# Performance work log

Hardware: AMD Instinct MI355X
Metric: run time of the kernel (lower is better)

## Reference

```python
import jax, jax.numpy as jnp
import numpy as np

B, C, L = 16, 256, 2048


def setup_inputs() -> dict:
    key = jax.random.key(0)
    ks = jax.random.split(key, 7)
    s = 0.05
    return {
        "x": jax.random.normal(ks[0], (B, C, L), dtype=jnp.float32),
        "W_theta": jax.random.normal(ks[1], (C, C), dtype=jnp.float32) * s,
        "b_theta": jax.random.normal(ks[2], (C,), dtype=jnp.float32) * s,
        "W_phi": jax.random.normal(ks[3], (C, C), dtype=jnp.float32) * s,
        "b_phi": jax.random.normal(ks[4], (C,), dtype=jnp.float32) * s,
        "W_g": jax.random.normal(ks[5], (C, C), dtype=jnp.float32) * s,
        "b_g": jax.random.normal(ks[6], (C,), dtype=jnp.float32) * s,
    }


def reference(x, W_theta, b_theta, W_phi, b_phi, W_g, b_g):
    # x: [B, C, L]; 1x1 Conv1d == linear over channel dim: out[b,o,l] = W[o,c] x[b,c,l] + b[o]
    q = jnp.einsum('oc,bcl->bol', W_theta, x) + b_theta[None, :, None]  # [B,C,L]
    k = jnp.einsum('oc,bcl->bol', W_phi, x) + b_phi[None, :, None]
    v = jnp.einsum('oc,bcl->bol', W_g, x) + b_g[None, :, None]
    num_c = x.shape[1]
    # scores[b,i,j] = sum_c q[b,c,i] * k[b,c,j]
    scores = jnp.einsum('bci,bcj->bij', q, k) / jnp.sqrt(jnp.float32(num_c))  # [B,L,L]
    attn = jax.nn.softmax(scores, axis=-1)
    # out[b,i,c] = sum_j attn[b,i,j] v[b,c,j]; then permute back to [B,C,L]
    attn_out = jnp.einsum('bij,bcj->bci', attn, v)  # [B,C,L]
    return x + attn_out
```

## Files before the change

### kernel.cpp

```cpp
#include <hip/hip_runtime.h>
#include <math.h>

#define B_ 16
#define C_ 256
#define L_ 2048

using short8 = __attribute__((ext_vector_type(8))) short;
using f32x4  = __attribute__((ext_vector_type(4))) float;

__device__ __forceinline__ unsigned short f2bf(float f) {
  unsigned u = __float_as_uint(f);
  return (unsigned short)((u + 0x7FFFu + ((u >> 16) & 1u)) >> 16);
}

__device__ __forceinline__ void gload16(const void* src, void* dst) {
  __builtin_amdgcn_global_load_lds(
      (const __attribute__((address_space(1))) unsigned int*)src,
      (__attribute__((address_space(3))) unsigned int*)dst, 16, 0, 0);
}

__global__ __launch_bounds__(256) void convert_w(const float* __restrict__ wt,
                                                 const float* __restrict__ wp,
                                                 const float* __restrict__ wg,
                                                 unsigned short* __restrict__ dst) {
  int i = blockIdx.x * 256 + threadIdx.x;
  dst[i]          = f2bf(wt[i]);
  dst[65536 + i]  = f2bf(wp[i]);
  dst[131072 + i] = f2bf(wg[i]);
}

__global__ __launch_bounds__(256, 2) void proj_kernel(
    const float* __restrict__ x, const unsigned short* __restrict__ wbf,
    const float* __restrict__ bth, const float* __restrict__ bph,
    const float* __restrict__ bg,
    unsigned short* __restrict__ qT, unsigned short* __restrict__ kT,
    unsigned short* __restrict__ vv)
{
  const int tid  = threadIdx.x;
  const int w    = tid >> 6;
  const int lane = tid & 63;
  const int r    = lane & 15;
  const int g    = lane >> 4;
  const int l0   = blockIdx.x * 64;
  const int b    = blockIdx.y;
  const int p    = blockIdx.z;

  __shared__ unsigned short xs[64 * 64];
  __shared__ unsigned short wsd[256 * 64];

  const unsigned short* wsrc = wbf + p * 65536;

  f32x4 acc[4][4];
#pragma unroll
  for (int mi = 0; mi < 4; ++mi)
#pragma unroll
    for (int ni = 0; ni < 4; ++ni) acc[mi][ni] = f32x4{0.f, 0.f, 0.f, 0.f};

  for (int ks = 0; ks < 4; ++ks) {
    __syncthreads();
#pragma unroll
    for (int it = 0; it < 8; ++it) {
      int d  = it * 256 + w * 64 + lane;
      int o  = d >> 3;
      int cs = d & 7;
      const unsigned short* src = wsrc + o * C_ + ks * 64 + ((cs ^ (o & 7)) << 3);
      gload16(src, (void*)(wsd + (size_t)(it * 256 + w * 64) * 8));
    }
#pragma unroll
    for (int it = 0; it < 16; ++it) {
      int l = (tid & 15) + 16 * (it & 3);
      int c = (tid >> 4) + 16 * (it >> 2);
      float xvv = x[((size_t)b * C_ + ks * 64 + c) * L_ + l0 + l];
      xs[l * 64 + (((c >> 3) ^ (l & 7)) << 3) + (c & 7)] = f2bf(xvv);
    }
    __syncthreads();

#pragma unroll
    for (int kk2 = 0; kk2 < 2; ++kk2) {
      short8 xf[4], wf[4];
#pragma unroll
      for (int i = 0; i < 4; ++i) {
        int lrow = 16 * i + r;
        xf[i] = *(const short8*)(xs + lrow * 64 + (((kk2 * 4 + g) ^ (lrow & 7)) << 3));
        int orow = 64 * w + 16 * i + r;
        wf[i] = *(const short8*)(wsd + orow * 64 + (((kk2 * 4 + g) ^ (orow & 7)) << 3));
      }
      if (p < 2) {
#pragma unroll
        for (int mi = 0; mi < 4; ++mi)
#pragma unroll
          for (int ni = 0; ni < 4; ++ni)
            acc[mi][ni] = __builtin_amdgcn_mfma_f32_16x16x32_bf16(xf[mi], wf[ni], acc[mi][ni], 0, 0, 0);
      } else {
#pragma unroll
        for (int mi = 0; mi < 4; ++mi)
#pragma unroll
          for (int ni = 0; ni < 4; ++ni)
            acc[mi][ni] = __builtin_amdgcn_mfma_f32_16x16x32_bf16(wf[mi], xf[ni], acc[mi][ni], 0, 0, 0);
      }
    }
  }

  if (p < 2) {
    unsigned short* dst = (p == 0) ? qT : kT;
    const float* bias   = (p == 0) ? bth : bph;
    const float scale   = (p == 0) ? 0.09016844005556021f : 1.0f;
#pragma unroll
    for (int ni = 0; ni < 4; ++ni) {
      int o    = 64 * w + 16 * ni + r;
      float bv = bias[o];
#pragma unroll
      for (int mi = 0; mi < 4; ++mi)
#pragma unroll
        for (int rr = 0; rr < 4; ++rr) {
          int l = l0 + 16 * mi + 4 * g + rr;
          dst[((size_t)b * L_ + l) * C_ + o] = f2bf((acc[mi][ni][rr] + bv) * scale);
        }
    }
  } else {
#pragma unroll
    for (int mi = 0; mi < 4; ++mi)
#pragma unroll
      for (int rr = 0; rr < 4; ++rr) {
        int o    = 64 * w + 16 * mi + 4 * g + rr;
        float bv = bg[o];
#pragma unroll
        for (int ni = 0; ni < 4; ++ni) {
          int l = l0 + 16 * ni + r;
          vv[((size_t)b * C_ + o) * L_ + l] = f2bf(acc[mi][ni][rr] + bv);
        }
      }
  }
}

__global__ __launch_bounds__(256, 2) void attn_kernel(
    const unsigned short* __restrict__ qT, const unsigned short* __restrict__ kT,
    const unsigned short* __restrict__ vv,
    const float* __restrict__ x, float* __restrict__ out)
{
  const int tid  = threadIdx.x;
  const int w    = tid >> 6;
  const int lane = tid & 63;
  const int r    = lane & 15;
  const int g    = lane >> 4;

  int wg = ((blockIdx.x & 7) << 6) | (blockIdx.x >> 3);
  const int i0 = (wg & 31) * 64;
  const int b  = wg >> 5;

  __shared__ unsigned short kls[64 * 256];
  __shared__ unsigned short vls[256 * 64];
  __shared__ unsigned short pls[64 * 64];
  __shared__ float lsums[64];

  short8 qf[8];
  const int qrow = i0 + 16 * w + r;
#pragma unroll
  for (int kk = 0; kk < 8; ++kk)
    qf[kk] = *(const short8*)(qT + ((size_t)b * L_ + qrow) * C_ + kk * 32 + 8 * g);

  f32x4 oacc[4][4];
#pragma unroll
  for (int mi = 0; mi < 4; ++mi)
#pragma unroll
    for (int nf = 0; nf < 4; ++nf) oacc[mi][nf] = f32x4{0.f, 0.f, 0.f, 0.f};
  float lsum[4] = {0.f, 0.f, 0.f, 0.f};

  const unsigned short* kTb = kT + (size_t)b * L_ * C_;
  const unsigned short* vvb = vv + (size_t)b * C_ * L_;

  for (int jt = 0; jt < 32; ++jt) {
    const int j0 = jt * 64;
    __syncthreads();
#pragma unroll
    for (int it = 0; it < 8; ++it) {
      int d   = it * 256 + w * 64 + lane;
      int row = d >> 5;
      int cs  = d & 31;
      const unsigned short* src = kTb + (size_t)(j0 + row) * C_ + ((cs ^ (row & 7)) << 3);
      gload16(src, (void*)(kls + (size_t)(it * 256 + w * 64) * 8));
    }
#pragma unroll
    for (int it = 0; it < 8; ++it) {
      int d   = it * 256 + w * 64 + lane;
      int row = d >> 3;
      int cs  = d & 7;
      const unsigned short* src = vvb + (size_t)row * L_ + j0 + ((cs ^ (row & 7)) << 3);
      gload16(src, (void*)(vls + (size_t)(it * 256 + w * 64) * 8));
    }
    __syncthreads();

    f32x4 sacc[4];
#pragma unroll
    for (int ni = 0; ni < 4; ++ni) sacc[ni] = f32x4{0.f, 0.f, 0.f, 0.f};
#pragma unroll
    for (int kk = 0; kk < 8; ++kk) {
#pragma unroll
      for (int ni = 0; ni < 4; ++ni) {
        int jrow = 16 * ni + r;
        short8 kf = *(const short8*)(kls + jrow * 256 + (((4 * kk + g) ^ (jrow & 7)) << 3));
        sacc[ni] = __builtin_amdgcn_mfma_f32_16x16x32_bf16(qf[kk], kf, sacc[ni], 0, 0, 0);
      }
    }

#pragma unroll
    for (int ni = 0; ni < 4; ++ni) {
#pragma unroll
      for (int rr = 0; rr < 4; ++rr) {
        float pv = exp2f(sacc[ni][rr]);
        lsum[rr] += pv;
        int irow = 16 * w + 4 * g + rr;
        int j    = r + 16 * ni;
        pls[irow * 64 + (((j >> 3) ^ (irow & 7)) << 3) + (j & 7)] = f2bf(pv);
      }
    }
    __syncthreads();

#pragma unroll
    for (int kk2 = 0; kk2 < 2; ++kk2) {
      short8 pf[4];
#pragma unroll
      for (int mi = 0; mi < 4; ++mi) {
        int irow = 16 * mi + r;
        pf[mi] = *(const short8*)(pls + irow * 64 + (((4 * kk2 + g) ^ (irow & 7)) << 3));
      }
#pragma unroll
      for (int nf = 0; nf < 4; ++nf) {
        int crow = 64 * w + 16 * nf + r;
        short8 vf = *(const short8*)(vls + crow * 64 + (((4 * kk2 + g) ^ (crow & 7)) << 3));
#pragma unroll
        for (int mi = 0; mi < 4; ++mi)
          oacc[mi][nf] = __builtin_amdgcn_mfma_f32_16x16x32_bf16(pf[mi], vf, oacc[mi][nf], 0, 0, 0);
      }
    }
  }

#pragma unroll
  for (int off = 1; off < 16; off <<= 1)
#pragma unroll
    for (int rr = 0; rr < 4; ++rr) lsum[rr] += __shfl_xor(lsum[rr], off);
  if (r == 0) {
    f32x4 t{lsum[0], lsum[1], lsum[2], lsum[3]};
    *(f32x4*)(lsums + 16 * w + 4 * g) = t;
  }
  __syncthreads();

#pragma unroll
  for (int mi = 0; mi < 4; ++mi) {
    f32x4 ls = *(const f32x4*)(lsums + 16 * mi + 4 * g);
    f32x4 linv;
#pragma unroll
    for (int rr = 0; rr < 4; ++rr) linv[rr] = 1.0f / ls[rr];
#pragma unroll
    for (int nf = 0; nf < 4; ++nf) {
      int c = 64 * w + 16 * nf + r;
      size_t base = ((size_t)b * C_ + c) * L_ + i0 + 16 * mi + 4 * g;
      f32x4 xv = *(const f32x4*)(x + base);
      f32x4 ov;
#pragma unroll
      for (int rr = 0; rr < 4; ++rr) ov[rr] = xv[rr] + oacc[mi][nf][rr] * linv[rr];
      *(f32x4*)(out + base) = ov;
    }
  }
}

extern "C" void kernel_launch(void* const* d_in, const int* in_sizes, int n_in,
                              void* d_out, int out_size, void* d_ws, size_t ws_size,
                              hipStream_t stream) {
  (void)in_sizes; (void)n_in; (void)out_size; (void)ws_size;
  const float* x   = (const float*)d_in[0];
  const float* wt  = (const float*)d_in[1];
  const float* bt  = (const float*)d_in[2];
  const float* wp  = (const float*)d_in[3];
  const float* bp  = (const float*)d_in[4];
  const float* wg  = (const float*)d_in[5];
  const float* bgg = (const float*)d_in[6];
  float* out = (float*)d_out;

  char* ws = (char*)d_ws;
  unsigned short* wbf = (unsigned short*)ws;
  unsigned short* qT  = (unsigned short*)(ws + 393216);
  unsigned short* kT  = (unsigned short*)(ws + 393216 + 16777216);
  unsigned short* vv  = (unsigned short*)(ws + 393216 + 2 * 16777216);

  convert_w<<<dim3(256), dim3(256), 0, stream>>>(wt, wp, wg, wbf);
  proj_kernel<<<dim3(32, 16, 3), dim3(256), 0, stream>>>(x, wbf, bt, bp, bgg, qT, kT, vv);
  attn_kernel<<<dim3(512), dim3(256), 0, stream>>>(qT, kT, vv, x, out);
}
```

Before: 140.1 us.

## Switch attention to 32x32x16 MFMA, prefetch K tiles, load V directly

Rewrites the attention kernel to use 32x32x16 bf16 MFMA tiles, with each wave computing a 32x32 score block split over i and j halves. The next K tile is prefetched into LDS while the P·V product runs. V fragments are now read straight from global memory into registers, which drops the V LDS buffer and its staging. This cuts LDS traffic and synchronization per tile. In exchange it uses more registers for Q fragments and accumulators, and the global V reads now sit on the critical path.

```diff
diff --git a/kernel.cpp b/kernel.cpp
--- a/kernel.cpp
+++ b/kernel.cpp
@@ -7,6 +7,8 @@
 
 using short8 = __attribute__((ext_vector_type(8))) short;
 using f32x4  = __attribute__((ext_vector_type(4))) float;
+using f32x16 = __attribute__((ext_vector_type(16))) float;
+typedef unsigned int uint;
 
 __device__ __forceinline__ unsigned short f2bf(float f) {
   unsigned u = __float_as_uint(f);
@@ -141,127 +143,140 @@
   const int tid  = threadIdx.x;
   const int w    = tid >> 6;
   const int lane = tid & 63;
-  const int r    = lane & 15;
-  const int g    = lane >> 4;
+  const int l31  = lane & 31;
+  const int hi   = lane >> 5;
+  const int ih   = w >> 1;
+  const int jh   = w & 1;
 
   int wg = ((blockIdx.x & 7) << 6) | (blockIdx.x >> 3);
   const int i0 = (wg & 31) * 64;
   const int b  = wg >> 5;
 
   __shared__ unsigned short kls[64 * 256];
-  __shared__ unsigned short vls[256 * 64];
   __shared__ unsigned short pls[64 * 64];
-  __shared__ float lsums[64];
-
-  short8 qf[8];
-  const int qrow = i0 + 16 * w + r;
-#pragma unroll
-  for (int kk = 0; kk < 8; ++kk)
-    qf[kk] = *(const short8*)(qT + ((size_t)b * L_ + qrow) * C_ + kk * 32 + 8 * g);
-
-  f32x4 oacc[4][4];
-#pragma unroll
-  for (int mi = 0; mi < 4; ++mi)
-#pragma unroll
-    for (int nf = 0; nf < 4; ++nf) oacc[mi][nf] = f32x4{0.f, 0.f, 0.f, 0.f};
-  float lsum[4] = {0.f, 0.f, 0.f, 0.f};
+  __shared__ float lsums2[2][64];
+
+  short8 qf[16];
+  const unsigned short* qrow_p = qT + ((size_t)b * L_ + i0 + 32 * ih + l31) * C_;
+#pragma unroll
+  for (int ks = 0; ks < 16; ++ks)
+    qf[ks] = *(const short8*)(qrow_p + ks * 16 + 8 * hi);
+
+  f32x16 oacc[2][2];
+#pragma unroll
+  for (int it = 0; it < 2; ++it)
+#pragma unroll
+    for (int ct = 0; ct < 2; ++ct)
+#pragma unroll
+      for (int e = 0; e < 16; ++e) oacc[it][ct][e] = 0.f;
+  float lsum = 0.f;
 
   const unsigned short* kTb = kT + (size_t)b * L_ * C_;
   const unsigned short* vvb = vv + (size_t)b * C_ * L_;
+
+#pragma unroll
+  for (int it = 0; it < 8; ++it) {
+    int d   = it * 256 + w * 64 + lane;
+    int row = d >> 5;
+    int cs  = d & 31;
+    gload16(kTb + (size_t)row * C_ + ((cs ^ (row & 7)) << 3),
+            (void*)(kls + (size_t)(it * 256 + w * 64) * 8));
+  }
 
   for (int jt = 0; jt < 32; ++jt) {
     const int j0 = jt * 64;
     __syncthreads();
-#pragma unroll
-    for (int it = 0; it < 8; ++it) {
-      int d   = it * 256 + w * 64 + lane;
-      int row = d >> 5;
-      int cs  = d & 31;
-      const unsigned short* src = kTb + (size_t)(j0 + row) * C_ + ((cs ^ (row & 7)) << 3);
-      gload16(src, (void*)(kls + (size_t)(it * 256 + w * 64) * 8));
-    }
-#pragma unroll
-    for (int it = 0; it < 8; ++it) {
-      int d   = it * 256 + w * 64 + lane;
-      int row = d >> 3;
-      int cs  = d & 7;
-      const unsigned short* src = vvb + (size_t)row * L_ + j0 + ((cs ^ (row & 7)) << 3);
-      gload16(src, (void*)(vls + (size_t)(it * 256 + w * 64) * 8));
+
+    f32x16 sacc;
+#pragma unroll
+    for (int e = 0; e < 16; ++e) sacc[e] = 0.f;
+    const int jrow = l31 + 32 * jh;
+#pragma unroll
+    for (int ks = 0; ks < 16; ++ks) {
+      short8 kf = *(const short8*)(kls + jrow * 256 + (((2 * ks + hi) ^ (jrow & 7)) << 3));
+      sacc = __builtin_amdgcn_mfma_f32_32x32x16_bf16(kf, qf[ks], sacc, 0, 0, 0);
+    }
+
+    {
+      const int i = l31 + 32 * ih;
+#pragma unroll
+      for (int q = 0; q < 4; ++q) {
+        float p0 = exp2f(sacc[4 * q + 0]);
+        float p1 = exp2f(sacc[4 * q + 1]);
+        float p2 = exp2f(sacc[4 * q + 2]);
+        float p3 = exp2f(sacc[4 * q + 3]);
+        lsum += (p0 + p1) + (p2 + p3);
+        uint2 d2;
+        d2.x = (uint)f2bf(p0) | ((uint)f2bf(p1) << 16);
+        d2.y = (uint)f2bf(p2) | ((uint)f2bf(p3) << 16);
+        int slot = (4 * jh + q) ^ (i & 7);
+        *(uint2*)(pls + i * 64 + slot * 8 + 4 * hi) = d2;
+      }
     }
     __syncthreads();
 
-    f32x4 sacc[4];
-#pragma unroll
-    for (int ni = 0; ni < 4; ++ni) sacc[ni] = f32x4{0.f, 0.f, 0.f, 0.f};
-#pragma unroll
-    for (int kk = 0; kk < 8; ++kk) {
-#pragma unroll
-      for (int ni = 0; ni < 4; ++ni) {
-        int jrow = 16 * ni + r;
-        short8 kf = *(const short8*)(kls + jrow * 256 + (((4 * kk + g) ^ (jrow & 7)) << 3));
-        sacc[ni] = __builtin_amdgcn_mfma_f32_16x16x32_bf16(qf[kk], kf, sacc[ni], 0, 0, 0);
-      }
-    }
-
-#pragma unroll
-    for (int ni = 0; ni < 4; ++ni) {
-#pragma unroll
-      for (int rr = 0; rr < 4; ++rr) {
-        float pv = exp2f(sacc[ni][rr]);
-        lsum[rr] += pv;
-        int irow = 16 * w + 4 * g + rr;
-        int j    = r + 16 * ni;
-        pls[irow * 64 + (((j >> 3) ^ (irow & 7)) << 3) + (j & 7)] = f2bf(pv);
-      }
-    }
-    __syncthreads();
-
-#pragma unroll
-    for (int kk2 = 0; kk2 < 2; ++kk2) {
-      short8 pf[4];
-#pragma unroll
-      for (int mi = 0; mi < 4; ++mi) {
-        int irow = 16 * mi + r;
-        pf[mi] = *(const short8*)(pls + irow * 64 + (((4 * kk2 + g) ^ (irow & 7)) << 3));
-      }
-#pragma unroll
-      for (int nf = 0; nf < 4; ++nf) {
-        int crow = 64 * w + 16 * nf + r;
-        short8 vf = *(const short8*)(vls + crow * 64 + (((4 * kk2 + g) ^ (crow & 7)) << 3));
-#pragma unroll
-        for (int mi = 0; mi < 4; ++mi)
-          oacc[mi][nf] = __builtin_amdgcn_mfma_f32_16x16x32_bf16(pf[mi], vf, oacc[mi][nf], 0, 0, 0);
-      }
+    if (jt < 31) {
+#pragma unroll
+      for (int it = 0; it < 8; ++it) {
+        int d   = it * 256 + w * 64 + lane;
+        int row = d >> 5;
+        int cs  = d & 31;
+        gload16(kTb + (size_t)(j0 + 64 + row) * C_ + ((cs ^ (row & 7)) << 3),
+                (void*)(kls + (size_t)(it * 256 + w * 64) * 8));
+      }
+    }
+
+    short8 vfr[2][4];
+#pragma unroll
+    for (int ct = 0; ct < 2; ++ct) {
+      const unsigned short* vrow = vvb + (size_t)(l31 + 32 * ct + 64 * w) * L_ + j0 + 8 * hi;
+#pragma unroll
+      for (int ks = 0; ks < 4; ++ks)
+        vfr[ct][ks] = *(const short8*)(vrow + 16 * ks);
+    }
+
+#pragma unroll
+    for (int ks = 0; ks < 4; ++ks) {
+      short8 pf[2];
+#pragma unroll
+      for (int it = 0; it < 2; ++it) {
+        int irow = l31 + 32 * it;
+        pf[it] = *(const short8*)(pls + irow * 64 + (((2 * ks + hi) ^ (irow & 7)) << 3));
+      }
+#pragma unroll
+      for (int it = 0; it < 2; ++it)
+#pragma unroll
+        for (int ct = 0; ct < 2; ++ct)
+          oacc[it][ct] = __builtin_amdgcn_mfma_f32_32x32x16_bf16(pf[it], vfr[ct][ks], oacc[it][ct], 0, 0, 0);
     }
   }
 
-#pragma unroll
-  for (int off = 1; off < 16; off <<= 1)
-#pragma unroll
-    for (int rr = 0; rr < 4; ++rr) lsum[rr] += __shfl_xor(lsum[rr], off);
-  if (r == 0) {
-    f32x4 t{lsum[0], lsum[1], lsum[2], lsum[3]};
-    *(f32x4*)(lsums + 16 * w + 4 * g) = t;
-  }
+  lsum += __shfl_xor(lsum, 32);
+  if (lane < 32) lsums2[jh][32 * ih + l31] = lsum;
   __syncthreads();
 
 #pragma unroll
-  for (int mi = 0; mi < 4; ++mi) {
-    f32x4 ls = *(const f32x4*)(lsums + 16 * mi + 4 * g);
-    f32x4 linv;
-#pragma unroll
-    for (int rr = 0; rr < 4; ++rr) linv[rr] = 1.0f / ls[rr];
-#pragma unroll
-    for (int nf = 0; nf < 4; ++nf) {
-      int c = 64 * w + 16 * nf + r;
-      size_t base = ((size_t)b * C_ + c) * L_ + i0 + 16 * mi + 4 * g;
-      f32x4 xv = *(const f32x4*)(x + base);
-      f32x4 ov;
-#pragma unroll
-      for (int rr = 0; rr < 4; ++rr) ov[rr] = xv[rr] + oacc[mi][nf][rr] * linv[rr];
-      *(f32x4*)(out + base) = ov;
-    }
-  }
+  for (int it = 0; it < 2; ++it)
+#pragma unroll
+    for (int q = 0; q < 4; ++q) {
+      int ib = 32 * it + 8 * q + 4 * hi;
+      f32x4 ls0 = *(const f32x4*)(&lsums2[0][ib]);
+      f32x4 ls1 = *(const f32x4*)(&lsums2[1][ib]);
+      f32x4 linv;
+#pragma unroll
+      for (int rr = 0; rr < 4; ++rr) linv[rr] = 1.0f / (ls0[rr] + ls1[rr]);
+#pragma unroll
+      for (int ct = 0; ct < 2; ++ct) {
+        int c = l31 + 32 * ct + 64 * w;
+        size_t base = ((size_t)b * C_ + c) * L_ + i0 + ib;
+        f32x4 xv = *(const f32x4*)(x + base);
+        f32x4 ov;
+#pragma unroll
+        for (int rr = 0; rr < 4; ++rr)
+          ov[rr] = xv[rr] + oacc[it][ct][4 * q + rr] * linv[rr];
+        *(f32x4*)(out + base) = ov;
+      }
+    }
 }
 
 extern "C" void kernel_launch(void* const* d_in, const int* in_sizes, int n_in,
```

Result: slower. 158.8 us (+13.3%).
